# Kernel tuning notes

Measured on AMD Instinct MI355X. Metric: run time of the kernel, lower is better.

Reference implementation:

```python
import jax, jax.numpy as jnp
import numpy as np

B = 512
IN_CORES = 12      # input_eff_capsules = 3072/256
N_PRIM = 12        # num_primary_capsules
N_PAR = 10         # num_parent_capsules
RFPC = 4           # receptive fields per capsule = 256/64
RF = 64            # receptive field size
CAP = 256          # capsule size
P_CONN = 0.2


def setup_inputs() -> dict:
    key = jax.random.key(0)
    ks = jax.random.split(key, 16)
    x = jax.random.uniform(ks[0], (B, 32, 32, 3), dtype=jnp.float32)
    # sparse 0/1 routing tensors (fixed Bernoulli(p) connectivity, stored as float params)
    C1 = jax.random.bernoulli(ks[1], P_CONN, (IN_CORES, RFPC, N_PRIM, RFPC)).astype(jnp.float32)
    C_skip = jax.random.bernoulli(ks[2], P_CONN, (IN_CORES, RFPC, N_PAR, RFPC)).astype(jnp.float32)
    C2 = jax.random.bernoulli(ks[3], P_CONN, (N_PRIM, RFPC, N_PAR, RFPC)).astype(jnp.float32)
    # per-receptive-field linear weights of the capsule layers
    s = 1.0 / np.sqrt(RF)
    W1 = jax.random.normal(ks[4], (N_PRIM, RFPC, RF, RF), dtype=jnp.float32) * s
    b1 = jnp.zeros((N_PRIM, RFPC, RF), dtype=jnp.float32)
    W2 = jax.random.normal(ks[5], (N_PAR, RFPC, RF, RF), dtype=jnp.float32) * s
    b2 = jnp.zeros((N_PAR, RFPC, RF), dtype=jnp.float32)
    # reconstruction MLP: 2560 -> 5000 -> 4000 -> 3072
    Wr1 = jax.random.normal(ks[6], (2560, 5000), dtype=jnp.float32) * (1.0 / np.sqrt(2560))
    br1 = jnp.zeros((5000,), dtype=jnp.float32)
    Wr2 = jax.random.normal(ks[7], (5000, 4000), dtype=jnp.float32) * (1.0 / np.sqrt(5000))
    br2 = jnp.zeros((4000,), dtype=jnp.float32)
    Wr3 = jax.random.normal(ks[8], (4000, 3072), dtype=jnp.float32) * (1.0 / np.sqrt(4000))
    br3 = jnp.zeros((3072,), dtype=jnp.float32)
    return {"x": x, "C1": C1, "W1": W1, "b1": b1, "C_skip": C_skip,
            "C2": C2, "W2": W2, "b2": b2,
            "Wr1": Wr1, "br1": br1, "Wr2": Wr2, "br2": br2, "Wr3": Wr3, "br3": br3}


def _caps_layer(x_flat, C, W, b):
    # x_flat: (B, in_cores*RFPC*RF); C: (in_cores, RFPC, out_caps, RFPC)
    bsz = x_flat.shape[0]
    in_cores = C.shape[0]
    xr = x_flat.reshape(bsz, in_cores, RFPC, RF)
    routed = jnp.einsum('ijkl,bijm->bklm', C, xr)          # (B, out_caps, RFPC, RF)
    out = jax.nn.relu(jnp.einsum('bklm,klmn->bkln', routed, W) + b)
    return out.reshape(bsz, -1)


def reference(x, C1, W1, b1, C_skip, C2, W2, b2, Wr1, br1, Wr2, br2, Wr3, br3):
    bsz = x.shape[0]
    # spatial_block_reshape: pure reshapes -> flatten
    x_flat = x.reshape(bsz, -1)                             # (B, 3072)
    # primary capsule layer
    x_prim = _caps_layer(x_flat, C1, W1, b1)                # (B, 3072)
    # skip connection: sparse routing einsum input->parent
    xr = x_prim.reshape(bsz, IN_CORES, RFPC, RF)
    x_skip = jnp.einsum('ijkl,bijm->bklm', C_skip, xr).reshape(bsz, -1)  # (B, 2560)
    # parent capsule layer + skip
    x_sum = x_skip + _caps_layer(x_prim, C2, W2, b2)        # (B, 2560)
    # top-1 capsule mask by norm
    norms = jnp.linalg.norm(x_sum.reshape(bsz, N_PAR, CAP), axis=-1)  # (B, 10)
    active = jnp.argmax(norms, axis=-1)                     # (B,)
    cap_id = jnp.arange(N_PAR * CAP) // CAP                 # (2560,)
    mask = (cap_id[None, :] == active[:, None]).astype(x_sum.dtype)
    x_recon = mask * x_sum
    # reconstruction MLP
    h = jax.nn.relu(x_recon @ Wr1 + br1)
    h = jax.nn.relu(h @ Wr2 + br2)
    out = jax.nn.sigmoid(h @ Wr3 + br3)                     # (B, 3072)
    return (out, x_sum)
```

## Files before the change

### kernel.cpp

```cpp
#include <hip/hip_runtime.h>
#include <math.h>


#define BATCH 512
#define OUT0_SZ (512*3072)

typedef __attribute__((ext_vector_type(8))) short short8;
typedef __attribute__((ext_vector_type(4))) float f32x4;

__device__ inline unsigned short f2bf(float f) {
    union { float f; unsigned u; } v; v.f = f;
    unsigned r = v.u + 0x7fffu + ((v.u >> 16) & 1u);
    return (unsigned short)(r >> 16);
}
__device__ inline float bf2f(unsigned int hi16) {
    union { unsigned u; float f; } v; v.u = hi16 << 16; return v.f;
}

#define GLD16(g, l) __builtin_amdgcn_global_load_lds( \
    (const __attribute__((address_space(1))) unsigned int*)(g), \
    (__attribute__((address_space(3))) unsigned int*)(l), 16, 0, 0)

__global__ __launch_bounds__(256) void convT_all(
    const float* __restrict__ Wr1, unsigned short* __restrict__ Wt1,
    const float* __restrict__ Wr2, unsigned short* __restrict__ Wt2,
    const float* __restrict__ Wr3, unsigned short* __restrict__ Wt3,
    const float* __restrict__ W1,  unsigned short* __restrict__ W1t,
    const float* __restrict__ W2,  unsigned short* __restrict__ W2t)
{
    __shared__ float t[64 * 65];
    int bid = blockIdx.x;
    const float* W; unsigned short* Wt;
    int Kr, Nr, Kp, ktiles, rem;
    if (bid < 3200)       { W = Wr1; Wt = Wt1; Kr = 2560; Nr = 5000; Kp = 2560; ktiles = 40; rem = bid; }
    else if (bid < 8320)  { W = Wr2; Wt = Wt2; Kr = 5000; Nr = 4000; Kp = 5120; ktiles = 80; rem = bid - 3200; }
    else if (bid < 11392) { W = Wr3; Wt = Wt3; Kr = 4000; Nr = 3072; Kp = 4096; ktiles = 64; rem = bid - 8320; }
    else if (bid < 11440) { int kl = bid - 11392; W = W1 + (size_t)kl * 4096; Wt = W1t + (size_t)kl * 4096;
                            Kr = 64; Nr = 64; Kp = 64; ktiles = 1; rem = 0; }
    else                  { int kl = bid - 11440; W = W2 + (size_t)kl * 4096; Wt = W2t + (size_t)kl * 4096;
                            Kr = 64; Nr = 64; Kp = 64; ktiles = 1; rem = 0; }
    int k0 = (rem % ktiles) * 64;
    int n0 = (rem / ktiles) * 64;
    int tid = threadIdx.x;

    {
        int kr = tid >> 4;
        int nc = (tid & 15) * 4;
        #pragma unroll
        for (int p = 0; p < 4; ++p) {
            int k = k0 + kr + p * 16;
            float4 v = make_float4(0.f, 0.f, 0.f, 0.f);
            if (k < Kr) {
                if (n0 + nc + 3 < Nr) {
                    v = *(const float4*)&W[(size_t)k * Nr + n0 + nc];
                } else {
                    float tmp[4] = {0.f, 0.f, 0.f, 0.f};
                    #pragma unroll
                    for (int j = 0; j < 4; ++j)
                        if (n0 + nc + j < Nr) tmp[j] = W[(size_t)k * Nr + n0 + nc + j];
                    v = make_float4(tmp[0], tmp[1], tmp[2], tmp[3]);
                }
            }
            float* row = &t[(kr + p * 16) * 65 + nc];
            row[0] = v.x; row[1] = v.y; row[2] = v.z; row[3] = v.w;
        }
    }
    __syncthreads();
    {
        int nr = tid >> 2;
        int kc = (tid & 3) * 16;
        unsigned int u[8];
        #pragma unroll
        for (int j = 0; j < 8; ++j) {
            float v0 = t[(kc + 2 * j)     * 65 + nr];
            float v1 = t[(kc + 2 * j + 1) * 65 + nr];
            u[j] = (unsigned int)f2bf(v0) | ((unsigned int)f2bf(v1) << 16);
        }
        unsigned int* dst = (unsigned int*)&Wt[(size_t)(n0 + nr) * Kp + k0 + kc];
        *(uint4*)(dst)     = make_uint4(u[0], u[1], u[2], u[3]);
        *(uint4*)(dst + 4) = make_uint4(u[4], u[5], u[6], u[7]);
    }
}

__global__ __launch_bounds__(256) void caps_gemm1(
    const float* __restrict__ x, const float* __restrict__ C1,
    const unsigned short* __restrict__ W1t, const float* __restrict__ b1,
    unsigned short* __restrict__ xp)
{
    __shared__ __align__(16) unsigned short As[128 * 72];
    __shared__ __align__(16) unsigned short Bs[64 * 72];
    __shared__ float Csh[48];
    int kl = blockIdx.x;
    int bm = blockIdx.y * 128;
    int tid = threadIdx.x;
    int w = tid >> 6, lane = tid & 63, q = lane >> 4, r16 = lane & 15;
    int wm = (w >> 1) * 64, wn = (w & 1) * 32;

    if (tid < 48) Csh[tid] = C1[tid * 48 + kl];
    {
        const uint4* src = (const uint4*)(W1t + (size_t)kl * 4096);
        #pragma unroll
        for (int p = 0; p < 2; ++p) {
            int c = tid + p * 256;
            int row = c >> 3, cq = c & 7;
            *(uint4*)&Bs[row * 72 + cq * 8] = src[c];
        }
    }
    __syncthreads();

    int arow = tid >> 1, ah = (tid & 1) * 32;
    float accp[32];
    #pragma unroll
    for (int i = 0; i < 32; ++i) accp[i] = 0.f;
    const float* xrow = x + (size_t)(bm + arow) * 3072 + ah;
    for (int ij = 0; ij < 48; ++ij) {
        float c = Csh[ij];
        if (c != 0.f) {
            const float4* p4 = (const float4*)(xrow + ij * 64);
            #pragma unroll
            for (int cc = 0; cc < 8; ++cc) {
                float4 v = p4[cc];
                accp[cc * 4 + 0] = fmaf(c, v.x, accp[cc * 4 + 0]);
                accp[cc * 4 + 1] = fmaf(c, v.y, accp[cc * 4 + 1]);
                accp[cc * 4 + 2] = fmaf(c, v.z, accp[cc * 4 + 2]);
                accp[cc * 4 + 3] = fmaf(c, v.w, accp[cc * 4 + 3]);
            }
        }
    }
    {
        unsigned short* dst = &As[arow * 72 + ah];
        #pragma unroll
        for (int cc = 0; cc < 4; ++cc) {
            unsigned int u[4];
            #pragma unroll
            for (int j = 0; j < 4; ++j)
                u[j] = (unsigned int)f2bf(accp[cc * 8 + 2 * j]) |
                       ((unsigned int)f2bf(accp[cc * 8 + 2 * j + 1]) << 16);
            *(uint4*)&dst[cc * 8] = make_uint4(u[0], u[1], u[2], u[3]);
        }
    }
    __syncthreads();

    f32x4 acc[4][2];
    #pragma unroll
    for (int i = 0; i < 4; ++i)
        #pragma unroll
        for (int j = 0; j < 2; ++j) acc[i][j] = (f32x4)0.f;
    #pragma unroll
    for (int ks = 0; ks < 2; ++ks) {
        short8 a[4], b[2];
        #pragma unroll
        for (int mt = 0; mt < 4; ++mt)
            a[mt] = *(const short8*)&As[(wm + mt * 16 + r16) * 72 + ks * 32 + q * 8];
        #pragma unroll
        for (int nt = 0; nt < 2; ++nt)
            b[nt] = *(const short8*)&Bs[(wn + nt * 16 + r16) * 72 + ks * 32 + q * 8];
        #pragma unroll
        for (int mt = 0; mt < 4; ++mt)
            #pragma unroll
            for (int nt = 0; nt < 2; ++nt)
                acc[mt][nt] = __builtin_amdgcn_mfma_f32_16x16x32_bf16(a[mt], b[nt], acc[mt][nt], 0, 0, 0);
    }

    #pragma unroll
    for (int mt = 0; mt < 4; ++mt) {
        #pragma unroll
        for (int nt = 0; nt < 2; ++nt) {
            int n = wn + nt * 16 + r16;
            float bv = b1[kl * 64 + n];
            #pragma unroll
            for (int reg = 0; reg < 4; ++reg) {
                int row = bm + wm + mt * 16 + q * 4 + reg;
                xp[(size_t)row * 3072 + kl * 64 + n] = f2bf(fmaxf(acc[mt][nt][reg] + bv, 0.f));
            }
        }
    }
}

__global__ __launch_bounds__(256) void caps_gemm2(
    const unsigned short* __restrict__ xp, const float* __restrict__ Cs,
    const float* __restrict__ C2, const unsigned short* __restrict__ W2t,
    const float* __restrict__ b2, float* __restrict__ xsum,
    float* __restrict__ part8)
{
    __shared__ __align__(16) unsigned short As[128 * 72];
    __shared__ __align__(16) unsigned short Bs[64 * 72];
    __shared__ __align__(16) float Sk[128 * 68];
    __shared__ float C2sh[48], Cssh[48];
    int kl = blockIdx.x;
    int bm = blockIdx.y * 128;
    int tid = threadIdx.x;
    int w = tid >> 6, lane = tid & 63, q = lane >> 4, r16 = lane & 15;
    int wm = (w >> 1) * 64, wn = (w & 1) * 32;
    int half = w & 1;

    if (tid < 48) { C2sh[tid] = C2[tid * 40 + kl]; Cssh[tid] = Cs[tid * 40 + kl]; }
    {
        const uint4* src = (const uint4*)(W2t + (size_t)kl * 4096);
        #pragma unroll
        for (int p = 0; p < 2; ++p) {
            int c = tid + p * 256;
            int row = c >> 3, cq = c & 7;
            *(uint4*)&Bs[row * 72 + cq * 8] = src[c];
        }
    }
    __syncthreads();

    int arow = tid >> 1, ah = (tid & 1) * 32;
    float accp[32], skp[32];
    #pragma unroll
    for (int i = 0; i < 32; ++i) { accp[i] = 0.f; skp[i] = 0.f; }
    const unsigned short* xprow = xp + (size_t)(bm + arow) * 3072 + ah;
    for (int ij = 0; ij < 48; ++ij) {
        float c2 = C2sh[ij], cs = Cssh[ij];
        if (c2 != 0.f || cs != 0.f) {
            const uint4* p4 = (const uint4*)(xprow + ij * 64);
            #pragma unroll
            for (int cc = 0; cc < 4; ++cc) {
                uint4 v = p4[cc];
                unsigned int uu[4] = {v.x, v.y, v.z, v.w};
                #pragma unroll
                for (int j = 0; j < 4; ++j) {
                    float lo = bf2f(uu[j] & 0xffffu);
                    float hi = bf2f(uu[j] >> 16);
                    int idx = cc * 8 + 2 * j;
                    accp[idx]     = fmaf(c2, lo, accp[idx]);
                    accp[idx + 1] = fmaf(c2, hi, accp[idx + 1]);
                    skp[idx]      = fmaf(cs, lo, skp[idx]);
                    skp[idx + 1]  = fmaf(cs, hi, skp[idx + 1]);
                }
            }
        }
    }
    {
        unsigned short* dst = &As[arow * 72 + ah];
        #pragma unroll
        for (int cc = 0; cc < 4; ++cc) {
            unsigned int u[4];
            #pragma unroll
            for (int j = 0; j < 4; ++j)
                u[j] = (unsigned int)f2bf(accp[cc * 8 + 2 * j]) |
                       ((unsigned int)f2bf(accp[cc * 8 + 2 * j + 1]) << 16);
            *(uint4*)&dst[cc * 8] = make_uint4(u[0], u[1], u[2], u[3]);
        }
        float* sdst = &Sk[arow * 68 + ah];
        #pragma unroll
        for (int cc = 0; cc < 8; ++cc)
            *(float4*)&sdst[cc * 4] = make_float4(skp[cc*4], skp[cc*4+1], skp[cc*4+2], skp[cc*4+3]);
    }
    __syncthreads();

    f32x4 acc[4][2];
    #pragma unroll
    for (int i = 0; i < 4; ++i)
        #pragma unroll
        for (int j = 0; j < 2; ++j) acc[i][j] = (f32x4)0.f;
    #pragma unroll
    for (int ks = 0; ks < 2; ++ks) {
        short8 a[4], b[2];
        #pragma unroll
        for (int mt = 0; mt < 4; ++mt)
            a[mt] = *(const short8*)&As[(wm + mt * 16 + r16) * 72 + ks * 32 + q * 8];
        #pragma unroll
        for (int nt = 0; nt < 2; ++nt)
            b[nt] = *(const short8*)&Bs[(wn + nt * 16 + r16) * 72 + ks * 32 + q * 8];
        #pragma unroll
        for (int mt = 0; mt < 4; ++mt)
            #pragma unroll
            for (int nt = 0; nt < 2; ++nt)
                acc[mt][nt] = __builtin_amdgcn_mfma_f32_16x16x32_bf16(a[mt], b[nt], acc[mt][nt], 0, 0, 0);
    }

    #pragma unroll
    for (int mt = 0; mt < 4; ++mt) {
        float sreg[4] = {0.f, 0.f, 0.f, 0.f};
        #pragma unroll
        for (int nt = 0; nt < 2; ++nt) {
            int n = wn + nt * 16 + r16;
            float bv = b2[kl * 64 + n];
            #pragma unroll
            for (int reg = 0; reg < 4; ++reg) {
                int lr = wm + mt * 16 + q * 4 + reg;
                float v = Sk[lr * 68 + n] + fmaxf(acc[mt][nt][reg] + bv, 0.f);
                xsum[(size_t)(bm + lr) * 2560 + kl * 64 + n] = v;
                sreg[reg] += v * v;
            }
        }
        #pragma unroll
        for (int reg = 0; reg < 4; ++reg) {
            float s = sreg[reg];
            s += __shfl_xor(s, 1); s += __shfl_xor(s, 2);
            s += __shfl_xor(s, 4); s += __shfl_xor(s, 8);
            if (r16 == 0) {
                int row = bm + wm + mt * 16 + q * 4 + reg;
                part8[(size_t)row * 80 + kl * 2 + half] = s;
            }
        }
    }
}

__global__ __launch_bounds__(256) void mask_kernel(
    const float* __restrict__ xs, const float* __restrict__ part8,
    unsigned short* __restrict__ xrec)
{
    int b = blockIdx.x;
    int tid = threadIdx.x;
    __shared__ float norms[10];
    __shared__ int act_sh;
    if (tid < 10) {
        float s = 0.f;
        #pragma unroll
        for (int j = 0; j < 8; ++j) s += part8[(size_t)b * 80 + tid * 8 + j];
        norms[tid] = s;
    }
    __syncthreads();
    if (tid == 0) {
        int best = 0; float bn = -1.f;
        #pragma unroll
        for (int k = 0; k < 10; ++k)
            if (norms[k] > bn) { bn = norms[k]; best = k; }
        act_sh = best;
    }
    __syncthreads();
    int act = act_sh;
    const float* xb = xs + (size_t)b * 2560;
    unsigned short* xr = xrec + (size_t)b * 2560;
    #pragma unroll
    for (int k = 0; k < 10; ++k) {
        int idx = k * 256 + tid;
        xr[idx] = (k == act) ? f2bf(xb[idx]) : (unsigned short)0;
    }
}

#define SPLITK 4
__global__ __launch_bounds__(256) void gemm_splitk(
    const unsigned short* __restrict__ A, int ldA,
    const unsigned short* __restrict__ Bt, int ldB,
    float* __restrict__ P, int Np, int kper)
{
    __shared__ __align__(16) unsigned short As[64 * 32];
    __shared__ __align__(16) unsigned short Bs[128 * 32];

    int tid = threadIdx.x;
    int bn = blockIdx.x * 128;
    int bm = blockIdx.y * 64;
    int kz = blockIdx.z * kper;

    int w = tid >> 6, lane = tid & 63;
    int wm = (w >> 1) * 32, wn = (w & 1) * 64;
    int q = lane >> 4, r16 = lane & 15;

    int srow = tid >> 2, skq = tid & 3;

    f32x4 acc[2][4];
    #pragma unroll
    for (int i = 0; i < 2; ++i)
        #pragma unroll
        for (int j = 0; j < 4; ++j) acc[i][j] = (f32x4)0.f;

    for (int kk = 0; kk < kper; kk += 32) {
        int k0 = kz + kk;
        const unsigned short* ga = A + (size_t)(bm + srow) * ldA + k0 + skq * 8;
        GLD16(ga, &As[tid * 8]);
        const unsigned short* gb = Bt + (size_t)(bn + srow) * ldB + k0 + skq * 8;
        GLD16(gb, &Bs[tid * 8]);
        GLD16(gb + (size_t)64 * ldB, &Bs[(tid + 256) * 8]);
        __syncthreads();

        short8 a[2], b[4];
        #pragma unroll
        for (int mt = 0; mt < 2; ++mt)
            a[mt] = *(const short8*)&As[(wm + mt * 16 + r16) * 32 + q * 8];
        #pragma unroll
        for (int nt = 0; nt < 4; ++nt)
            b[nt] = *(const short8*)&Bs[(wn + nt * 16 + r16) * 32 + q * 8];
        #pragma unroll
        for (int mt = 0; mt < 2; ++mt)
            #pragma unroll
            for (int nt = 0; nt < 4; ++nt)
                acc[mt][nt] = __builtin_amdgcn_mfma_f32_16x16x32_bf16(a[mt], b[nt], acc[mt][nt], 0, 0, 0);
        __syncthreads();
    }

    float* Pz = P + (size_t)blockIdx.z * 512 * Np;
    #pragma unroll
    for (int mt = 0; mt < 2; ++mt) {
        #pragma unroll
        for (int nt = 0; nt < 4; ++nt) {
            int cn = bn + wn + nt * 16 + r16;
            #pragma unroll
            for (int reg = 0; reg < 4; ++reg) {
                int cm = bm + wm + mt * 16 + q * 4 + reg;
                Pz[(size_t)cm * Np + cn] = acc[mt][nt][reg];
            }
        }
    }
}

template<int MODE>
__global__ __launch_bounds__(256) void combine_kernel(
    const float* __restrict__ P, const float* __restrict__ bias,
    void* __restrict__ out, int Np, int N_real)
{
    int gid = blockIdx.x * 256 + threadIdx.x;
    int n0 = (gid * 4) % Np;
    int m  = (gid * 4) / Np;
    size_t MN = (size_t)512 * Np;
    const float* p = P + (size_t)m * Np + n0;
    f32x4 s = *(const f32x4*)p;
    s += *(const f32x4*)(p + MN);
    s += *(const f32x4*)(p + 2 * MN);
    s += *(const f32x4*)(p + 3 * MN);
    f32x4 bv = (n0 < N_real) ? *(const f32x4*)(bias + n0) : (f32x4)0.f;
    s += bv;
    if (MODE == 0) {
        unsigned int lo = (unsigned int)f2bf(fmaxf(s[0], 0.f)) | ((unsigned int)f2bf(fmaxf(s[1], 0.f)) << 16);
        unsigned int hi = (unsigned int)f2bf(fmaxf(s[2], 0.f)) | ((unsigned int)f2bf(fmaxf(s[3], 0.f)) << 16);
        *(uint2*)((unsigned short*)out + (size_t)m * Np + n0) = make_uint2(lo, hi);
    } else {
        f32x4 v;
        v[0] = 1.f / (1.f + expf(-s[0]));
        v[1] = 1.f / (1.f + expf(-s[1]));
        v[2] = 1.f / (1.f + expf(-s[2]));
        v[3] = 1.f / (1.f + expf(-s[3]));
        *(f32x4*)((float*)out + (size_t)m * Np + n0) = v;
    }
}

extern "C" void kernel_launch(void* const* d_in, const int* in_sizes, int n_in,
                              void* d_out, int out_size, void* d_ws, size_t ws_size,
                              hipStream_t stream) {
    const float* x   = (const float*)d_in[0];
    const float* C1  = (const float*)d_in[1];
    const float* W1  = (const float*)d_in[2];
    const float* b1  = (const float*)d_in[3];
    const float* Cs  = (const float*)d_in[4];
    const float* C2  = (const float*)d_in[5];
    const float* W2  = (const float*)d_in[6];
    const float* b2  = (const float*)d_in[7];
    const float* Wr1 = (const float*)d_in[8];
    const float* br1 = (const float*)d_in[9];
    const float* Wr2 = (const float*)d_in[10];
    const float* br2 = (const float*)d_in[11];
    const float* Wr3 = (const float*)d_in[12];
    const float* br3 = (const float*)d_in[13];

    float* out = (float*)d_out;
    float* out0     = out;
    float* xsum_out = out + OUT0_SZ;

    char* base = (char*)d_ws;
    unsigned short* xrec  = (unsigned short*)(base);
    unsigned short* h1    = (unsigned short*)(base +   2621440);
    unsigned short* h2    = (unsigned short*)(base +   7864320);
    unsigned short* Wt1   = (unsigned short*)(base +  12058624);
    unsigned short* Wt2   = (unsigned short*)(base +  38273024);
    unsigned short* Wt3   = (unsigned short*)(base +  80216064);
    float*          Pbuf  = (float*)(base + 105381888);
    unsigned short* xp    = (unsigned short*)(base + 147324928);
    unsigned short* W1t   = (unsigned short*)(base + 150470656);
    unsigned short* W2t   = (unsigned short*)(base + 150863872);
    float*          part8 = (float*)(base + 151191552);

    convT_all<<<11480, 256, 0, stream>>>(Wr1, Wt1, Wr2, Wt2, Wr3, Wt3,
                                         W1, W1t, W2, W2t);

    caps_gemm1<<<dim3(48, 4), 256, 0, stream>>>(x, C1, W1t, b1, xp);
    caps_gemm2<<<dim3(40, 4), 256, 0, stream>>>(xp, Cs, C2, W2t, b2, xsum_out, part8);
    mask_kernel<<<BATCH, 256, 0, stream>>>(xsum_out, part8, xrec);

    gemm_splitk<<<dim3(5120 / 128, 8, SPLITK), 256, 0, stream>>>(xrec, 2560, Wt1, 2560, Pbuf, 5120, 2560 / SPLITK);
    combine_kernel<0><<<512 * 5120 / 1024, 256, 0, stream>>>(Pbuf, br1, h1, 5120, 5000);

    gemm_splitk<<<dim3(4096 / 128, 8, SPLITK), 256, 0, stream>>>(h1, 5120, Wt2, 5120, Pbuf, 4096, 5120 / SPLITK);
    combine_kernel<0><<<512 * 4096 / 1024, 256, 0, stream>>>(Pbuf, br2, h2, 4096, 4000);

    gemm_splitk<<<dim3(3072 / 128, 8, SPLITK), 256, 0, stream>>>(h2, 4096, Wt3, 4096, Pbuf, 3072, 4096 / SPLITK);
    combine_kernel<1><<<512 * 3072 / 1024, 256, 0, stream>>>(Pbuf, br3, out0, 3072, 3072);
}
```

Before: 409.2 us.

## Exploit top-1 capsule mask to shrink first MLP GEMM via row bucketing

The top-1 mask zeroes all but one 256-wide capsule per row. The new code buckets batch rows by their active capsule and runs a dedicated first-layer GEMM over only that 256-wide K slice. This replaces the full split-K GEMM and its combine pass. Row order is permuted through layers 2 and 3 and restored when the final sigmoid output is written. Separately, the weight transpose/convert kernel now handles four tiles per block with a double-buffered LDS load, to cut block count and overlap loads with packing.

```diff
diff --git a/kernel.cpp b/kernel.cpp
--- a/kernel.cpp
+++ b/kernel.cpp
@@ -20,6 +20,79 @@
 #define GLD16(g, l) __builtin_amdgcn_global_load_lds( \
     (const __attribute__((address_space(1))) unsigned int*)(g), \
     (__attribute__((address_space(3))) unsigned int*)(l), 16, 0, 0)
+
+struct CTJob {
+    const float* W; unsigned short* Wt;
+    int Kr, Nr, Kp, k0, n0;
+};
+
+__device__ inline CTJob ct_resolve(int bid,
+    const float* Wr1, unsigned short* Wt1,
+    const float* Wr2, unsigned short* Wt2,
+    const float* Wr3, unsigned short* Wt3,
+    const float* W1,  unsigned short* W1t,
+    const float* W2,  unsigned short* W2t)
+{
+    CTJob j;
+    int ktiles, rem;
+    if (bid < 3200)       { j.W = Wr1; j.Wt = Wt1; j.Kr = 2560; j.Nr = 5000; j.Kp = 2560; ktiles = 40; rem = bid; }
+    else if (bid < 8320)  { j.W = Wr2; j.Wt = Wt2; j.Kr = 5000; j.Nr = 4000; j.Kp = 5120; ktiles = 80; rem = bid - 3200; }
+    else if (bid < 11392) { j.W = Wr3; j.Wt = Wt3; j.Kr = 4000; j.Nr = 3072; j.Kp = 4096; ktiles = 64; rem = bid - 8320; }
+    else if (bid < 11440) { int kl = bid - 11392; j.W = W1 + (size_t)kl * 4096; j.Wt = W1t + (size_t)kl * 4096;
+                            j.Kr = 64; j.Nr = 64; j.Kp = 64; ktiles = 1; rem = 0; }
+    else                  { int kl = bid - 11440; j.W = W2 + (size_t)kl * 4096; j.Wt = W2t + (size_t)kl * 4096;
+                            j.Kr = 64; j.Nr = 64; j.Kp = 64; ktiles = 1; rem = 0; }
+    j.k0 = (rem % ktiles) * 64;
+    j.n0 = (rem / ktiles) * 64;
+    return j;
+}
+
+__device__ inline void ct_load(const CTJob& j, int tid, float4* v) {
+    int kr = tid >> 4;
+    int nc = (tid & 15) * 4;
+    #pragma unroll
+    for (int p = 0; p < 4; ++p) {
+        int k = j.k0 + kr + p * 16;
+        float4 vv = make_float4(0.f, 0.f, 0.f, 0.f);
+        if (k < j.Kr) {
+            if (j.n0 + nc + 3 < j.Nr) {
+                vv = *(const float4*)&j.W[(size_t)k * j.Nr + j.n0 + nc];
+            } else {
+                float tmp[4] = {0.f, 0.f, 0.f, 0.f};
+                #pragma unroll
+                for (int jj = 0; jj < 4; ++jj)
+                    if (j.n0 + nc + jj < j.Nr) tmp[jj] = j.W[(size_t)k * j.Nr + j.n0 + nc + jj];
+                vv = make_float4(tmp[0], tmp[1], tmp[2], tmp[3]);
+            }
+        }
+        v[p] = vv;
+    }
+}
+
+__device__ inline void ct_stlds(float* t, int tid, const float4* v) {
+    int kr = tid >> 4;
+    int nc = (tid & 15) * 4;
+    #pragma unroll
+    for (int p = 0; p < 4; ++p) {
+        float* row = &t[(kr + p * 16) * 65 + nc];
+        row[0] = v[p].x; row[1] = v[p].y; row[2] = v[p].z; row[3] = v[p].w;
+    }
+}
+
+__device__ inline void ct_pack(const CTJob& j, const float* t, int tid) {
+    int nr = tid >> 2;
+    int kc = (tid & 3) * 16;
+    unsigned int u[8];
+    #pragma unroll
+    for (int jj = 0; jj < 8; ++jj) {
+        float v0 = t[(kc + 2 * jj)     * 65 + nr];
+        float v1 = t[(kc + 2 * jj + 1) * 65 + nr];
+        u[jj] = (unsigned int)f2bf(v0) | ((unsigned int)f2bf(v1) << 16);
+    }
+    unsigned int* dst = (unsigned int*)&j.Wt[(size_t)(j.n0 + nr) * j.Kp + j.k0 + kc];
+    *(uint4*)(dst)     = make_uint4(u[0], u[1], u[2], u[3]);
+    *(uint4*)(dst + 4) = make_uint4(u[4], u[5], u[6], u[7]);
+}
 
 __global__ __launch_bounds__(256) void convT_all(
     const float* __restrict__ Wr1, unsigned short* __restrict__ Wt1,
@@ -28,57 +101,30 @@
     const float* __restrict__ W1,  unsigned short* __restrict__ W1t,
     const float* __restrict__ W2,  unsigned short* __restrict__ W2t)
 {
-    __shared__ float t[64 * 65];
-    int bid = blockIdx.x;
-    const float* W; unsigned short* Wt;
-    int Kr, Nr, Kp, ktiles, rem;
-    if (bid < 3200)       { W = Wr1; Wt = Wt1; Kr = 2560; Nr = 5000; Kp = 2560; ktiles = 40; rem = bid; }
-    else if (bid < 8320)  { W = Wr2; Wt = Wt2; Kr = 5000; Nr = 4000; Kp = 5120; ktiles = 80; rem = bid - 3200; }
-    else if (bid < 11392) { W = Wr3; Wt = Wt3; Kr = 4000; Nr = 3072; Kp = 4096; ktiles = 64; rem = bid - 8320; }
-    else if (bid < 11440) { int kl = bid - 11392; W = W1 + (size_t)kl * 4096; Wt = W1t + (size_t)kl * 4096;
-                            Kr = 64; Nr = 64; Kp = 64; ktiles = 1; rem = 0; }
-    else                  { int kl = bid - 11440; W = W2 + (size_t)kl * 4096; Wt = W2t + (size_t)kl * 4096;
-                            Kr = 64; Nr = 64; Kp = 64; ktiles = 1; rem = 0; }
-    int k0 = (rem % ktiles) * 64;
-    int n0 = (rem / ktiles) * 64;
+    __shared__ float t[2][64 * 65];
     int tid = threadIdx.x;
-
-    {
-        int kr = tid >> 4;
-        int nc = (tid & 15) * 4;
-        #pragma unroll
-        for (int p = 0; p < 4; ++p) {
-            int k = k0 + kr + p * 16;
-            float4 v = make_float4(0.f, 0.f, 0.f, 0.f);
-            if (k < Kr) {
-                if (n0 + nc + 3 < Nr) {
-                    v = *(const float4*)&W[(size_t)k * Nr + n0 + nc];
-                } else {
-                    float tmp[4] = {0.f, 0.f, 0.f, 0.f};
-                    #pragma unroll
-                    for (int j = 0; j < 4; ++j)
-                        if (n0 + nc + j < Nr) tmp[j] = W[(size_t)k * Nr + n0 + nc + j];
-                    v = make_float4(tmp[0], tmp[1], tmp[2], tmp[3]);
-                }
-            }
-            float* row = &t[(kr + p * 16) * 65 + nc];
-            row[0] = v.x; row[1] = v.y; row[2] = v.z; row[3] = v.w;
-        }
-    }
-    __syncthreads();
-    {
-        int nr = tid >> 2;
-        int kc = (tid & 3) * 16;
-        unsigned int u[8];
-        #pragma unroll
-        for (int j = 0; j < 8; ++j) {
-            float v0 = t[(kc + 2 * j)     * 65 + nr];
-            float v1 = t[(kc + 2 * j + 1) * 65 + nr];
-            u[j] = (unsigned int)f2bf(v0) | ((unsigned int)f2bf(v1) << 16);
-        }
-        unsigned int* dst = (unsigned int*)&Wt[(size_t)(n0 + nr) * Kp + k0 + kc];
-        *(uint4*)(dst)     = make_uint4(u[0], u[1], u[2], u[3]);
-        *(uint4*)(dst + 4) = make_uint4(u[4], u[5], u[6], u[7]);
+    int tbase = blockIdx.x * 4;
+
+    CTJob jc = ct_resolve(tbase, Wr1, Wt1, Wr2, Wt2, Wr3, Wt3, W1, W1t, W2, W2t);
+    float4 v[4];
+    ct_load(jc, tid, v);
+    ct_stlds(t[0], tid, v);
+    __syncthreads();
+
+    #pragma unroll
+    for (int i = 0; i < 4; ++i) {
+        CTJob jn;
+        float4 vn[4];
+        if (i < 3) {
+            jn = ct_resolve(tbase + i + 1, Wr1, Wt1, Wr2, Wt2, Wr3, Wt3, W1, W1t, W2, W2t);
+            ct_load(jn, tid, vn);
+        }
+        ct_pack(jc, t[i & 1], tid);
+        if (i < 3) {
+            ct_stlds(t[(i + 1) & 1], tid, vn);
+            jc = jn;
+        }
+        __syncthreads();
     }
 }
 
@@ -301,7 +347,7 @@
 
 __global__ __launch_bounds__(256) void mask_kernel(
     const float* __restrict__ xs, const float* __restrict__ part8,
-    unsigned short* __restrict__ xrec)
+    unsigned short* __restrict__ xrec, int* __restrict__ active)
 {
     int b = blockIdx.x;
     int tid = threadIdx.x;
@@ -320,15 +366,108 @@
         for (int k = 0; k < 10; ++k)
             if (norms[k] > bn) { bn = norms[k]; best = k; }
         act_sh = best;
+        active[b] = best;
     }
     __syncthreads();
     int act = act_sh;
-    const float* xb = xs + (size_t)b * 2560;
-    unsigned short* xr = xrec + (size_t)b * 2560;
-    #pragma unroll
-    for (int k = 0; k < 10; ++k) {
-        int idx = k * 256 + tid;
-        xr[idx] = (k == act) ? f2bf(xb[idx]) : (unsigned short)0;
+    int idx = act * 256 + tid;
+    xrec[(size_t)b * 2560 + idx] = f2bf(xs[(size_t)b * 2560 + idx]);
+}
+
+__global__ __launch_bounds__(512) void bucket_kernel(
+    const int* __restrict__ active, int* __restrict__ perm,
+    int4* __restrict__ slots)
+{
+    __shared__ int cnt[10], pos[10];
+    int tid = threadIdx.x;
+    if (tid < 10) cnt[tid] = 0;
+    __syncthreads();
+    int a = active[tid];
+    atomicAdd(&cnt[a], 1);
+    __syncthreads();
+    if (tid == 0) {
+        int o = 0, s = 0;
+        for (int g = 0; g < 10; ++g) {
+            pos[g] = o;
+            int mg = cnt[g];
+            for (int t0 = 0; t0 < mg; t0 += 64)
+                slots[s++] = make_int4(g, o + t0, min(64, mg - t0), 0);
+            o += mg;
+        }
+        for (; s < 18; ++s) slots[s] = make_int4(0, 0, 0, 0);
+    }
+    __syncthreads();
+    int r = atomicAdd(&pos[a], 1);
+    perm[r] = tid;
+}
+
+__global__ __launch_bounds__(256) void gemm_l1(
+    const unsigned short* __restrict__ xrec, const int* __restrict__ perm,
+    const int4* __restrict__ slots, const unsigned short* __restrict__ Wt1,
+    const float* __restrict__ br1, unsigned short* __restrict__ h1)
+{
+    int4 s = slots[blockIdx.y];
+    if (s.z == 0) return;
+    int g = s.x, mstart = s.y, mval = s.z;
+    int bn = blockIdx.x * 128;
+    int tid = threadIdx.x;
+
+    __shared__ __align__(16) unsigned short As[64 * 32];
+    __shared__ __align__(16) unsigned short Bs[128 * 32];
+    __shared__ int rows[64];
+    if (tid < 64) rows[tid] = perm[mstart + min(tid, mval - 1)];
+    __syncthreads();
+
+    int w = tid >> 6, lane = tid & 63;
+    int wm = (w >> 1) * 32, wn = (w & 1) * 64;
+    int q = lane >> 4, r16 = lane & 15;
+    int srow = tid >> 2, skq = tid & 3;
+
+    f32x4 acc[2][4];
+    #pragma unroll
+    for (int i = 0; i < 2; ++i)
+        #pragma unroll
+        for (int j = 0; j < 4; ++j) acc[i][j] = (f32x4)0.f;
+
+    int arow = rows[srow];
+    const unsigned short* ga = xrec + (size_t)arow * 2560 + g * 256 + skq * 8;
+    const unsigned short* gb = Wt1 + (size_t)(bn + srow) * 2560 + g * 256 + skq * 8;
+
+    for (int kk = 0; kk < 256; kk += 32) {
+        GLD16(ga + kk, &As[tid * 8]);
+        GLD16(gb + kk, &Bs[tid * 8]);
+        GLD16(gb + kk + (size_t)64 * 2560, &Bs[(tid + 256) * 8]);
+        __syncthreads();
+
+        short8 a[2], b[4];
+        #pragma unroll
+        for (int mt = 0; mt < 2; ++mt)
+            a[mt] = *(const short8*)&As[(wm + mt * 16 + r16) * 32 + q * 8];
+        #pragma unroll
+        for (int nt = 0; nt < 4; ++nt)
+            b[nt] = *(const short8*)&Bs[(wn + nt * 16 + r16) * 32 + q * 8];
+        #pragma unroll
+        for (int mt = 0; mt < 2; ++mt)
+            #pragma unroll
+            for (int nt = 0; nt < 4; ++nt)
+                acc[mt][nt] = __builtin_amdgcn_mfma_f32_16x16x32_bf16(a[mt], b[nt], acc[mt][nt], 0, 0, 0);
+        __syncthreads();
+    }
+
+    #pragma unroll
+    for (int mt = 0; mt < 2; ++mt) {
+        #pragma unroll
+        for (int nt = 0; nt < 4; ++nt) {
+            int n = bn + wn + nt * 16 + r16;
+            float bv = (n < 5000) ? br1[n] : 0.f;
+            #pragma unroll
+            for (int reg = 0; reg < 4; ++reg) {
+                int lm = wm + mt * 16 + q * 4 + reg;
+                if (lm < mval)
+                    h1[(size_t)(mstart + lm) * 5120 + n] =
+                        f2bf(fmaxf(acc[mt][nt][reg] + bv, 0.f));
+            }
+        }
     }
 }
 
@@ -400,7 +539,7 @@
 template<int MODE>
 __global__ __launch_bounds__(256) void combine_kernel(
     const float* __restrict__ P, const float* __restrict__ bias,
-    void* __restrict__ out, int Np, int N_real)
+    void* __restrict__ out, int Np, int N_real, const int* __restrict__ perm)
 {
     int gid = blockIdx.x * 256 + threadIdx.x;
     int n0 = (gid * 4) % Np;
@@ -418,12 +557,13 @@
         unsigned int hi = (unsigned int)f2bf(fmaxf(s[2], 0.f)) | ((unsigned int)f2bf(fmaxf(s[3], 0.f)) << 16);
         *(uint2*)((unsigned short*)out + (size_t)m * Np + n0) = make_uint2(lo, hi);
     } else {
+        int row = perm[m];
         f32x4 v;
         v[0] = 1.f / (1.f + expf(-s[0]));
         v[1] = 1.f / (1.f + expf(-s[1]));
         v[2] = 1.f / (1.f + expf(-s[2]));
         v[3] = 1.f / (1.f + expf(-s[3]));
-        *(f32x4*)((float*)out + (size_t)m * Np + n0) = v;
+        *(f32x4*)((float*)out + (size_t)row * Np + n0) = v;
     }
 }
 
@@ -461,20 +601,23 @@
     unsigned short* W1t   = (unsigned short*)(base + 150470656);
     unsigned short* W2t   = (unsigned short*)(base + 150863872);
     float*          part8 = (float*)(base + 151191552);
-
-    convT_all<<<11480, 256, 0, stream>>>(Wr1, Wt1, Wr2, Wt2, Wr3, Wt3,
-                                         W1, W1t, W2, W2t);
+    int*  active = (int*)(base + 105381888 + 33554432);
+    int*  perm   = active + 512;
+    int4* slots  = (int4*)(perm + 512);
+
+    convT_all<<<2870, 256, 0, stream>>>(Wr1, Wt1, Wr2, Wt2, Wr3, Wt3,
+                                        W1, W1t, W2, W2t);
 
     caps_gemm1<<<dim3(48, 4), 256, 0, stream>>>(x, C1, W1t, b1, xp);
     caps_gemm2<<<dim3(40, 4), 256, 0, stream>>>(xp, Cs, C2, W2t, b2, xsum_out, part8);
-    mask_kernel<<<BATCH, 256, 0, stream>>>(xsum_out, part8, xrec);
-
-    gemm_splitk<<<dim3(5120 / 128, 8, SPLITK), 256, 0, stream>>>(xrec, 2560, Wt1, 2560, Pbuf, 5120, 2560 / SPLITK);
-    combine_kernel<0><<<512 * 5120 / 1024, 256, 0, stream>>>(Pbuf, br1, h1, 5120, 5000);
+    mask_kernel<<<BATCH, 256, 0, stream>>>(xsum_out, part8, xrec, active);
+    bucket_kernel<<<1, 512, 0, stream>>>(active, perm, slots);
+
+    gemm_l1<<<dim3(5120 / 128, 18), 256, 0, stream>>>(xrec, perm, slots, Wt1, br1, h1);
 
     gemm_splitk<<<dim3(4096 / 128, 8, SPLITK), 256, 0, stream>>>(h1, 5120, Wt2, 5120, Pbuf, 4096, 5120 / SPLITK);
-    combine_kernel<0><<<512 * 4096 / 1024, 256, 0, stream>>>(Pbuf, br2, h2, 4096, 4000);
+    combine_kernel<0><<<512 * 4096 / 1024, 256, 0, stream>>>(Pbuf, br2, h2, 4096, 4000, nullptr);
 
     gemm_splitk<<<dim3(3072 / 128, 8, SPLITK), 256, 0, stream>>>(h2, 4096, Wt3, 4096, Pbuf, 3072, 4096 / SPLITK);
-    combine_kernel<1><<<512 * 3072 / 1024, 256, 0, stream>>>(Pbuf, br3, out0, 3072, 3072);
-}
+    combine_kernel<1><<<512 * 3072 / 1024, 256, 0, stream>>>(Pbuf, br3, out0, 3072, 3072, perm);
+}
```

Result: faster. 384.5 us (-6.0%).
